# Kernel tuning notes

Measured on AMD Instinct MI355X. Metric: run time of the kernel, lower is better.

The kernel has to match this reference:

```python
import jax, jax.numpy as jnp
import numpy as np

N = 100_000      # nodes
E = 1_600_000    # edges (avg degree 16)
IN_DIM = 256
HID = 128
N_OUT = 2


def _linear_params(key, fan_in, fan_out):
    kw, kb = jax.random.split(key)
    bound = 1.0 / np.sqrt(fan_in)
    W = jax.random.uniform(kw, (fan_in, fan_out), jnp.float32, -bound, bound)
    b = jax.random.uniform(kb, (fan_out,), jnp.float32, -bound, bound)
    return W, b


def setup_inputs() -> dict:
    key = jax.random.key(0)
    ks = jax.random.split(key, 6)
    edge_index = jax.random.randint(ks[0], (2, E), 0, N, dtype=jnp.int64)
    x = jax.random.normal(ks[1], (N, IN_DIM), jnp.float32)
    Wi, bi = _linear_params(ks[2], IN_DIM, HID)   # NodeInitializer.lin
    W1, b1 = _linear_params(ks[3], HID, HID)      # GCNConv 1
    W2, b2 = _linear_params(ks[4], HID, HID)      # GCNConv 2
    Wh, bh = _linear_params(ks[5], HID, N_OUT)    # head
    return {"edge_index": edge_index, "x": x, "Wi": Wi, "bi": bi,
            "W1": W1, "b1": b1, "W2": W2, "b2": b2, "Wh": Wh, "bh": bh}


def reference(edge_index, x, Wi, bi, W1, b1, W2, b2, Wh, bh):
    n = x.shape[0]
    # GCNConv preprocessing: add self-loops, symmetric degree normalization.
    loops = jnp.arange(n, dtype=edge_index.dtype)
    src = jnp.concatenate([edge_index[0], loops])  # message source
    dst = jnp.concatenate([edge_index[1], loops])  # aggregation target
    deg = jax.ops.segment_sum(jnp.ones(src.shape[0], jnp.float32), dst, num_segments=n)
    dinv = jnp.where(deg > 0, deg ** -0.5, 0.0)
    norm = dinv[src] * dinv[dst]                   # [E+N]

    # NodeInitializer: relu(linear(x)); dropout = identity (eval mode)
    h = jax.nn.relu(x @ Wi + bi)

    # Two GCNConv layers (no relu between, matching SimpleGCN.forward)
    for W, b in ((W1, b1), (W2, b2)):
        msg = (h @ W)[src] * norm[:, None]         # gather + normalize, [E+N, HID]
        h = jax.ops.segment_sum(msg, dst, num_segments=n) + b  # scatter-add

    return h @ Wh + bh                             # [N, N_OUT]
```

## Files before the change

kernel.cpp:

```cpp
#include <hip/hip_runtime.h>
#include <hip/hip_bf16.h>

#define N_NODES 100000
#define N_EDGES 1600000
#define DIM_IN  256
#define DIM_H   128

#define NBKT 782
#define CPAD 16
#define EPB  8192
#define NBLK ((N_EDGES + EPB - 1) / EPB)

typedef __attribute__((ext_vector_type(8))) short short8;
typedef __attribute__((ext_vector_type(4))) float f32x4;

__device__ __forceinline__ int get_src(const int* e, int is64, int i) {
  return is64 ? e[2 * i] : e[i];
}
__device__ __forceinline__ int get_dst(const int* e, int is64, int i) {
  return is64 ? e[2 * (N_EDGES + i)] : e[N_EDGES + i];
}

__global__ __launch_bounds__(1024)
void k_init(const int* __restrict__ e, int* __restrict__ flag,
            int* __restrict__ bcnt) {
  if (blockIdx.x == 0) {
    __shared__ int s;
    if (threadIdx.x == 0) s = 0;
    __syncthreads();
    atomicOr(&s, e[2 * threadIdx.x + 1]);
    __syncthreads();
    if (threadIdx.x == 0) *flag = (s == 0) ? 1 : 0;
  } else {
    int i = (blockIdx.x - 1) * 1024 + threadIdx.x;
    if (i < NBKT * CPAD) bcnt[i] = 0;
  }
}

__global__ __launch_bounds__(256) void k_zero(int* __restrict__ p, int n) {
  int i = blockIdx.x * 256 + threadIdx.x;
  if (i < n) p[i] = 0;
}

__global__ __launch_bounds__(1024)
void k_binc(const int* __restrict__ eidx, const int* __restrict__ flag,
            int* __restrict__ bcnt) {
  __shared__ int hist[NBKT];
  const int t = threadIdx.x;
  const int is64 = *flag;
  for (int i = t; i < NBKT; i += 1024) hist[i] = 0;
  __syncthreads();
#pragma unroll
  for (int j = 0; j < EPB / 1024; ++j) {
    int e = blockIdx.x * EPB + j * 1024 + t;
    if (e < N_EDGES) {
      unsigned s = (unsigned)get_src(eidx, is64, e);
      unsigned d = (unsigned)get_dst(eidx, is64, e);
      if (s < N_NODES && d < N_NODES) atomicAdd(&hist[d >> 7], 1);
    }
  }
  __syncthreads();
  for (int i = t; i < NBKT; i += 1024) {
    int h = hist[i];
    if (h) atomicAdd(&bcnt[i * CPAD], h);
  }
}

__global__ __launch_bounds__(1024)
void k_bscan(int* __restrict__ bcnt, int* __restrict__ bbase) {
  __shared__ int sm[1024];
  int t = threadIdx.x;
  int v = (t < NBKT) ? bcnt[t * CPAD] : 0;
  sm[t] = v;
  __syncthreads();
  for (int d = 1; d < 1024; d <<= 1) {
    int u = (t >= d) ? sm[t - d] : 0;
    __syncthreads();
    sm[t] += u;
    __syncthreads();
  }
  if (t < NBKT) {
    int excl = sm[t] - v;
    bbase[t] = excl;
    bcnt[t * CPAD] = excl;
    if (t == NBKT - 1) bbase[NBKT] = sm[t];
  }
}

__global__ __launch_bounds__(1024)
void k_bin(const int* __restrict__ eidx, const int* __restrict__ flag,
           int* __restrict__ bcnt, unsigned* __restrict__ ebuf) {
  __shared__ int hist[NBKT];
  __shared__ int cur[NBKT];
  const int t = threadIdx.x;
  const int is64 = *flag;
  for (int i = t; i < NBKT; i += 1024) hist[i] = 0;
  unsigned rec[EPB / 1024];
  int bkt[EPB / 1024];
  __syncthreads();
#pragma unroll
  for (int j = 0; j < EPB / 1024; ++j) {
    int e = blockIdx.x * EPB + j * 1024 + t;
    bkt[j] = -1;
    rec[j] = 0;
    if (e < N_EDGES) {
      unsigned s = (unsigned)get_src(eidx, is64, e);
      unsigned d = (unsigned)get_dst(eidx, is64, e);
      if (s < N_NODES && d < N_NODES) {
        bkt[j] = (int)(d >> 7);
        rec[j] = s | ((d & 127u) << 17);
        atomicAdd(&hist[bkt[j]], 1);
      }
    }
  }
  __syncthreads();
  for (int i = t; i < NBKT; i += 1024) {
    int h = hist[i];
    cur[i] = h ? atomicAdd(&bcnt[i * CPAD], h) : 0;
  }
  __syncthreads();
#pragma unroll
  for (int j = 0; j < EPB / 1024; ++j) {
    if (bkt[j] >= 0) {
      int pos = atomicAdd(&cur[bkt[j]], 1);
      ebuf[pos] = rec[j];
    }
  }
}

__global__ __launch_bounds__(256)
void k_csr(const int* __restrict__ bbase, const unsigned* __restrict__ ebuf,
           int* __restrict__ off, float* __restrict__ dinv,
           int* __restrict__ csr) {
  __shared__ int hist[128];
  __shared__ int scn[128];
  __shared__ int cur[128];
  const int b = blockIdx.x, t = threadIdx.x;
  const int n0 = b << 7;
  const int start = bbase[b], end = bbase[b + 1];
  if (t < 128) hist[t] = 0;
  __syncthreads();
  for (int i = start + t; i < end; i += 256) {
    atomicAdd(&hist[ebuf[i] >> 17], 1);
  }
  __syncthreads();
  if (t < 128) scn[t] = hist[t];
  __syncthreads();
  for (int d = 1; d < 128; d <<= 1) {
    int u = (t < 128 && t >= d) ? scn[t - d] : 0;
    __syncthreads();
    if (t < 128) scn[t] += u;
    __syncthreads();
  }
  if (t < 128) {
    int node = n0 + t;
    if (node < N_NODES) {
      off[node] = start + scn[t];
      dinv[node] = rsqrtf(1.0f + (float)hist[t]);
      cur[t] = start + scn[t] - hist[t];
    }
  }
  __syncthreads();
  for (int i = start + t; i < end; i += 256) {
    unsigned r = ebuf[i];
    int pos = atomicAdd(&cur[r >> 17], 1);
    csr[pos] = (int)(r & 0x1FFFFu);
  }
}

__device__ __forceinline__ ushort f2bf(float f) {
  unsigned u = __float_as_uint(f);
  unsigned r = (u + 0x7fffu + ((u >> 16) & 1u)) >> 16;
  return (ushort)r;
}
__device__ __forceinline__ float bf2f(ushort h) {
  return __uint_as_float(((unsigned)h) << 16);
}

__device__ __forceinline__ void load8(const float* p, float* o) {
  float4 a = reinterpret_cast<const float4*>(p)[0];
  float4 b = reinterpret_cast<const float4*>(p)[1];
  o[0] = a.x; o[1] = a.y; o[2] = a.z; o[3] = a.w;
  o[4] = b.x; o[5] = b.y; o[6] = b.z; o[7] = b.w;
}

__global__ __launch_bounds__(256)
void k_prep(const float* __restrict__ Wi, const float* __restrict__ W1,
            const float* __restrict__ W2, const float* __restrict__ Wh,
            const float* __restrict__ b1, const float* __restrict__ b2,
            const float* __restrict__ bh, ushort* __restrict__ outHi,
            float* __restrict__ Wcc) {
  __shared__ float Wc2s[DIM_H][2];
  constexpr int CH = DIM_IN / 32;
  if (blockIdx.x == 16) {
    const int t = threadIdx.x;
    const int i = t >> 1, j = t & 1;
    float s = 0.f;
#pragma unroll 4
    for (int m = 0; m < DIM_H; ++m) s += W2[(size_t)i * DIM_H + m] * Wh[m * 2 + j];
    Wc2s[i][j] = s;
    __syncthreads();
    float c = 0.f;
#pragma unroll 4
    for (int k = 0; k < DIM_H; ++k) c += W1[(size_t)i * DIM_H + k] * Wc2s[k][j];
    Wcc[i * 2 + j] = c;
    if (t < 2) {
      float a = 0.f, b = 0.f;
      for (int k = 0; k < DIM_H; ++k) {
        a += b1[k] * Wc2s[k][t];
        b += b2[k] * Wh[k * 2 + t];
      }
      Wcc[256 + t] = a;
      Wcc[258 + t] = b + bh[t];
    }
    return;
  }
  int idx = blockIdx.x * 256 + threadIdx.x;
  int n  = idx & 15;
  int qq = (idx >> 4) & 3;
  int nt = (idx >> 6) & 7;
  int c  = idx >> 9;
  int col = nt * 16 + n;
  short8 h8, l8;
#pragma unroll
  for (int j = 0; j < 8; ++j) {
    float v = Wi[(size_t)(c * 32 + qq * 8 + j) * DIM_H + col];
    ushort hb = f2bf(v);
    ushort lb = f2bf(v - bf2f(hb));
    h8[j] = (short)hb;
    l8[j] = (short)lb;
  }
  ((short8*)outHi)[idx] = h8;
  ((short8*)outHi)[CH * 512 + idx] = l8;
}

template <int K>
__global__ __launch_bounds__(256)
void k_gemm_xz(const float* __restrict__ A, const ushort* __restrict__ Bfrag,
               const float* __restrict__ bias, const float* __restrict__ Wcc,
               const float* __restrict__ dinv, float4* __restrict__ tbl) {
  constexpr int CH = K / 32;
  const int tid = threadIdx.x;
  const int wave = tid >> 6, lane = tid & 63;
  const int m_l = lane & 15, quad = lane >> 4;
  const int mrow = blockIdx.x * 64 + wave * 16;

  f32x4 acc[8];
#pragma unroll
  for (int nt = 0; nt < 8; ++nt) acc[nt] = (f32x4){0.f, 0.f, 0.f, 0.f};

  const short8* Bhi8 = (const short8*)Bfrag;
  const short8* Blo8 = Bhi8 + CH * 512;

  const int rowc = (mrow + m_l < N_NODES) ? (mrow + m_l) : (N_NODES - 1);
  const float* Ap = &A[(size_t)rowc * K + quad * 8];

#pragma unroll 2
  for (int c = 0; c < CH; ++c) {
    float v[8];
    load8(Ap + c * 32, v);
    short8 ahi, alo;
#pragma unroll
    for (int j = 0; j < 8; ++j) {
      ushort hb = f2bf(v[j]);
      ushort lb = f2bf(v[j] - bf2f(hb));
      ahi[j] = (short)hb;
      alo[j] = (short)lb;
    }
#pragma unroll
    for (int nt = 0; nt < 8; ++nt) {
      const int bent = ((c * 8 + nt) * 4 + quad) * 16 + m_l;
      short8 bhi = Bhi8[bent];
      short8 blo = Blo8[bent];
      acc[nt] = __builtin_amdgcn_mfma_f32_16x16x32_bf16(ahi, bhi, acc[nt], 0, 0, 0);
      acc[nt] = __builtin_amdgcn_mfma_f32_16x16x32_bf16(ahi, blo, acc[nt], 0, 0, 0);
      acc[nt] = __builtin_amdgcn_mfma_f32_16x16x32_bf16(alo, bhi, acc[nt], 0, 0, 0);
    }
  }

  float p0[4], p1[4];
#pragma unroll
  for (int r = 0; r < 4; ++r) { p0[r] = 0.f; p1[r] = 0.f; }
#pragma unroll
  for (int nt = 0; nt < 8; ++nt) {
    const int colg = nt * 16 + m_l;
    const float bv = bias[colg];
    const float w0 = Wcc[colg * 2 + 0];
    const float w1 = Wcc[colg * 2 + 1];
#pragma unroll
    for (int r = 0; r < 4; ++r) {
      float hv = fmaxf(acc[nt][r] + bv, 0.f);
      p0[r] += hv * w0;
      p1[r] += hv * w1;
    }
  }
#pragma unroll
  for (int o = 1; o < 16; o <<= 1) {
#pragma unroll
    for (int r = 0; r < 4; ++r) {
      p0[r] += __shfl_xor(p0[r], o);
      p1[r] += __shfl_xor(p1[r], o);
    }
  }
  if (m_l == 0) {
#pragma unroll
    for (int r = 0; r < 4; ++r) {
      const int rowg = mrow + quad * 4 + r;
      if (rowg < N_NODES) {
        float dn = dinv[rowg];
        tbl[rowg] = make_float4(dn * p0[r], dn * p1[r], dn, 0.f);
      }
    }
  }
}

__global__ __launch_bounds__(256)
void k_aggr1(const int* __restrict__ off, const int* __restrict__ csr,
             const float4* __restrict__ tbl, float2* __restrict__ tb2,
             float* __restrict__ g) {
  int node = blockIdx.x * 256 + threadIdx.x;
  if (node >= N_NODES) return;
  int start = (node == 0) ? 0 : off[node - 1];
  int end = off[node];
  float4 self = tbl[node];
  float s0 = self.x, s1 = self.y, sd = self.z;
  int e = start;
  for (; e + 3 < end; e += 4) {
    int i0 = csr[e], i1 = csr[e + 1], i2 = csr[e + 2], i3 = csr[e + 3];
    float4 v0 = tbl[i0];
    float4 v1 = tbl[i1];
    float4 v2 = tbl[i2];
    float4 v3 = tbl[i3];
    s0 += (v0.x + v1.x) + (v2.x + v3.x);
    s1 += (v0.y + v1.y) + (v2.y + v3.y);
    sd += (v0.z + v1.z) + (v2.z + v3.z);
  }
  for (; e < end; ++e) {
    float4 v = tbl[csr[e]];
    s0 += v.x; s1 += v.y; sd += v.z;
  }
  float dn = self.z;
  tb2[node] = make_float2(dn * dn * s0, dn * dn * s1);
  g[node] = dn * sd;
}

__global__ __launch_bounds__(256)
void k_aggr2(const int* __restrict__ off, const int* __restrict__ csr,
             const float2* __restrict__ tb2, const float* __restrict__ dinv,
             const float* __restrict__ g, const float* __restrict__ tail,
             float* __restrict__ out) {
  int node = blockIdx.x * 256 + threadIdx.x;
  if (node >= N_NODES) return;
  int start = (node == 0) ? 0 : off[node - 1];
  int end = off[node];
  float2 self = tb2[node];
  float s0 = self.x, s1 = self.y;
  int e = start;
  for (; e + 3 < end; e += 4) {
    int i0 = csr[e], i1 = csr[e + 1], i2 = csr[e + 2], i3 = csr[e + 3];
    float2 v0 = tb2[i0];
    float2 v1 = tb2[i1];
    float2 v2 = tb2[i2];
    float2 v3 = tb2[i3];
    s0 += (v0.x + v1.x) + (v2.x + v3.x);
    s1 += (v0.y + v1.y) + (v2.y + v3.y);
  }
  for (; e < end; ++e) {
    float2 v = tb2[csr[e]];
    s0 += v.x; s1 += v.y;
  }
  float dn = dinv[node], gv = g[node];
  float o0 = dn * s0 + gv * tail[0] + tail[2];
  float o1 = dn * s1 + gv * tail[1] + tail[3];
  reinterpret_cast<float2*>(out)[node] = make_float2(o0, o1);
}

__global__ __launch_bounds__(256) void k_count(const int* __restrict__ eidx,
                                               const int* __restrict__ flag,
                                               int* __restrict__ off) {
  int e = blockIdx.x * 256 + threadIdx.x;
  int is64 = *flag;
  if (e < N_EDGES) {
    unsigned d = (unsigned)get_dst(eidx, is64, e);
    if (d < N_NODES) atomicAdd(&off[d], 1);
  }
}

__global__ __launch_bounds__(256) void k_dinv_old(const int* __restrict__ off,
                                                  float* __restrict__ dinv) {
  int i = blockIdx.x * 256 + threadIdx.x;
  if (i < N_NODES) dinv[i] = rsqrtf(1.0f + (float)off[i]);
}

template <int K>
__global__ __launch_bounds__(256)
void k_gemm(const float* __restrict__ A, const float* __restrict__ B,
            const float* __restrict__ bias, const float* __restrict__ scale,
            float* __restrict__ C, const int do_relu) {
  __shared__ float As[64][33];
  const int tid = threadIdx.x;
  const int tx = tid & 15;
  const int ty = tid >> 4;
  const int m0 = blockIdx.x * 64;

  float acc[4][8];
#pragma unroll
  for (int i = 0; i < 4; ++i)
#pragma unroll
    for (int j = 0; j < 8; ++j) acc[i][j] = 0.f;

  const int rs = tid >> 2;
  const int ks = (tid & 3) * 8;

  for (int k0 = 0; k0 < K; k0 += 32) {
    float av8[8];
    const int gm = m0 + rs;
    if (gm < N_NODES) {
      load8(&A[(size_t)gm * K + k0 + ks], av8);
    } else {
#pragma unroll
      for (int j = 0; j < 8; ++j) av8[j] = 0.f;
    }
    __syncthreads();
#pragma unroll
    for (int j = 0; j < 8; ++j) As[rs][ks + j] = av8[j];
    __syncthreads();

    const float* Bp = B + (size_t)k0 * DIM_H + tx * 8;
#pragma unroll 4
    for (int k = 0; k < 32; ++k) {
      float bv[8];
      load8(Bp + (size_t)k * DIM_H, bv);
      float av[4];
#pragma unroll
      for (int rr = 0; rr < 4; ++rr) av[rr] = As[ty * 4 + rr][k];
#pragma unroll
      for (int rr = 0; rr < 4; ++rr)
#pragma unroll
        for (int cc = 0; cc < 8; ++cc)
          acc[rr][cc] = fmaf(av[rr], bv[cc], acc[rr][cc]);
    }
  }

  float bs[8];
  if (bias) {
    load8(bias + tx * 8, bs);
  } else {
#pragma unroll
    for (int j = 0; j < 8; ++j) bs[j] = 0.f;
  }
#pragma unroll
  for (int rr = 0; rr < 4; ++rr) {
    const int gm = m0 + ty * 4 + rr;
    if (gm < N_NODES) {
      float sc = scale ? scale[gm] : 1.0f;
      float v[8];
#pragma unroll
      for (int cc = 0; cc < 8; ++cc) {
        float t = acc[rr][cc] + bs[cc];
        if (do_relu) t = fmaxf(t, 0.f);
        v[cc] = t * sc;
      }
      float* Cp = &C[(size_t)gm * DIM_H + tx * 8];
      reinterpret_cast<float4*>(Cp)[0] = make_float4(v[0], v[1], v[2], v[3]);
      reinterpret_cast<float4*>(Cp)[1] = make_float4(v[4], v[5], v[6], v[7]);
    }
  }
}

__global__ __launch_bounds__(256)
void k_aggr_init(const float* __restrict__ t, const float* __restrict__ dinv,
                 const float* __restrict__ bias, float* __restrict__ h) {
  int idx = blockIdx.x * 256 + threadIdx.x;
  if (idx < N_NODES * DIM_H) {
    int i = idx >> 7;
    int c = idx & 127;
    float d = dinv[i];
    h[idx] = bias[c] + t[idx] * d * d;
  }
}

__global__ __launch_bounds__(256)
void k_aggr_edges(const int* __restrict__ eidx, const int* __restrict__ flag,
                  const float* __restrict__ t, const float* __restrict__ dinv,
                  float* __restrict__ h) {
  int e = blockIdx.x * 2 + (threadIdx.x >> 7);
  int c = threadIdx.x & 127;
  int is64 = *flag;
  if (e < N_EDGES) {
    unsigned s = (unsigned)get_src(eidx, is64, e);
    unsigned d = (unsigned)get_dst(eidx, is64, e);
    if (s < N_NODES && d < N_NODES) {
      float nrm = dinv[s] * dinv[d];
      unsafeAtomicAdd(&h[(size_t)d * DIM_H + c], t[(size_t)s * DIM_H + c] * nrm);
    }
  }
}

__global__ __launch_bounds__(256)
void k_head_f32(const float* __restrict__ h, const float* __restrict__ Wh,
                const float* __restrict__ bh, float* __restrict__ out) {
  int node = blockIdx.x * 4 + (threadIdx.x >> 6);
  int lane = threadIdx.x & 63;
  if (node >= N_NODES) return;
  float h0 = h[(size_t)node * DIM_H + lane];
  float h1 = h[(size_t)node * DIM_H + 64 + lane];
  float s0 = h0 * Wh[lane * 2 + 0] + h1 * Wh[(lane + 64) * 2 + 0];
  float s1 = h0 * Wh[lane * 2 + 1] + h1 * Wh[(lane + 64) * 2 + 1];
#pragma unroll
  for (int off = 32; off > 0; off >>= 1) {
    s0 += __shfl_down(s0, off);
    s1 += __shfl_down(s1, off);
  }
  if (lane == 0) {
    reinterpret_cast<float2*>(out)[node] = make_float2(s0 + bh[0], s1 + bh[1]);
  }
}

extern "C" void kernel_launch(void* const* d_in, const int* in_sizes, int n_in,
                              void* d_out, int out_size, void* d_ws, size_t ws_size,
                              hipStream_t stream) {
  (void)in_sizes; (void)n_in; (void)out_size;
  const int* eidx = (const int*)d_in[0];
  const float* x  = (const float*)d_in[1];
  const float* Wi = (const float*)d_in[2];
  const float* bi = (const float*)d_in[3];
  const float* W1 = (const float*)d_in[4];
  const float* b1 = (const float*)d_in[5];
  const float* W2 = (const float*)d_in[6];
  const float* b2 = (const float*)d_in[7];
  const float* Wh = (const float*)d_in[8];
  const float* bh = (const float*)d_in[9];
  float* out = (float*)d_out;

  const int gE  = (N_EDGES + 255) / 256;
  const int gM  = (N_NODES + 63) / 64;
  const int gW  = (N_NODES + 3) / 4;
  const int gN256 = (N_NODES + 255) / 256;

  char* ws = (char*)d_ws;
  int* flag = (int*)ws;

  const size_t need1 = 17410048;

  if (ws_size >= need1) {
    int*      bcnt  = (int*)(ws + 4096);
    int*      bbase = (int*)(ws + 57344);
    float*    Wcc   = (float*)(ws + 61440);
    ushort*   bfWi  = (ushort*)(ws + 65536);
    int*      off   = (int*)(ws + 262144);
    float*    dinv  = (float*)(ws + 720896);
    float*    g     = (float*)(ws + 1179648);
    float4*   tbl   = (float4*)(ws + 1638400);
    float2*   tb2   = (float2*)(ws + 3407872);
    int*      csr   = (int*)(ws + 4456448);
    unsigned* ebuf  = (unsigned*)(ws + 11010048);

    k_init<<<1 + (NBKT * CPAD + 1023) / 1024, 1024, 0, stream>>>(eidx, flag, bcnt);
    k_binc<<<NBLK, 1024, 0, stream>>>(eidx, flag, bcnt);
    k_bscan<<<1, 1024, 0, stream>>>(bcnt, bbase);
    k_bin<<<NBLK, 1024, 0, stream>>>(eidx, flag, bcnt, ebuf);
    k_csr<<<NBKT, 256, 0, stream>>>(bbase, ebuf, off, dinv, csr);

    k_prep<<<17, 256, 0, stream>>>(Wi, W1, W2, Wh, b1, b2, bh, bfWi, Wcc);

    k_gemm_xz<DIM_IN><<<gM, 256, 0, stream>>>(x, bfWi, bi, Wcc, dinv, tbl);
    k_aggr1<<<gN256, 256, 0, stream>>>(off, csr, tbl, tb2, g);
    k_aggr2<<<gN256, 256, 0, stream>>>(off, csr, tb2, dinv, g, Wcc + 256, out);
  } else {
    const int gN  = (N_NODES + 255) / 256;
    int*   off  = (int*)(ws + 4096);
    float* dinv = (float*)(ws + 404480);
    float* fbA  = (float*)(ws + 804864);
    float* fbB  = (float*)(ws + 804864 + (size_t)N_NODES * DIM_H * 4);
    const int gNH = (N_NODES * DIM_H + 255) / 256;
    const int gE2 = (N_EDGES + 1) / 2;
    k_init<<<1, 1024, 0, stream>>>(eidx, flag, (int*)(ws + 4096));
    k_zero<<<gN, 256, 0, stream>>>(off, N_NODES);
    k_count<<<gE, 256, 0, stream>>>(eidx, flag, off);
    k_dinv_old<<<gN, 256, 0, stream>>>(off, dinv);

    k_gemm<DIM_IN><<<gM, 256, 0, stream>>>(x, Wi, bi, nullptr, fbA, 1);
    k_gemm<DIM_H><<<gM, 256, 0, stream>>>(fbA, W1, nullptr, nullptr, fbB, 0);
    k_aggr_init<<<gNH, 256, 0, stream>>>(fbB, dinv, b1, fbA);
    k_aggr_edges<<<gE2, 256, 0, stream>>>(eidx, flag, fbB, dinv, fbA);
    k_gemm<DIM_H><<<gM, 256, 0, stream>>>(fbA, W2, nullptr, nullptr, fbB, 0);
    k_aggr_init<<<gNH, 256, 0, stream>>>(fbB, dinv, b2, fbA);
    k_aggr_edges<<<gE2, 256, 0, stream>>>(eidx, flag, fbB, dinv, fbA);
    k_head_f32<<<gW, 256, 0, stream>>>(fbA, Wh, bh, out);
  }
}
```

Baseline: 302.4 us.

## Restructure x@Wi GEMM: 128-row tiles, LDS double-buffered A, per-wave column split

Result: faster. 294.5 us (-2.6%).

```diff
diff --git a/kernel.cpp b/kernel.cpp
--- a/kernel.cpp
+++ b/kernel.cpp
@@ -182,6 +182,16 @@
   float4 b = reinterpret_cast<const float4*>(p)[1];
   o[0] = a.x; o[1] = a.y; o[2] = a.z; o[3] = a.w;
   o[4] = b.x; o[5] = b.y; o[6] = b.z; o[7] = b.w;
+}
+
+__device__ __forceinline__ void cvt_split(const float* v, short8& h, short8& l) {
+#pragma unroll
+  for (int j = 0; j < 8; ++j) {
+    ushort hb = f2bf(v[j]);
+    ushort lb = f2bf(v[j] - bf2f(hb));
+    h[j] = (short)hb;
+    l[j] = (short)lb;
+  }
 }
 
 __global__ __launch_bounds__(256)
@@ -235,81 +245,136 @@
 }
 
 template <int K>
-__global__ __launch_bounds__(256)
+__global__ __launch_bounds__(256, 3)
 void k_gemm_xz(const float* __restrict__ A, const ushort* __restrict__ Bfrag,
                const float* __restrict__ bias, const float* __restrict__ Wcc,
                const float* __restrict__ dinv, float4* __restrict__ tbl) {
   constexpr int CH = K / 32;
+  __shared__ __align__(16) ushort AhiS[2][512 * 8];
+  __shared__ __align__(16) ushort AloS[2][512 * 8];
   const int tid = threadIdx.x;
+  const int m0 = blockIdx.x * 128;
   const int wave = tid >> 6, lane = tid & 63;
   const int m_l = lane & 15, quad = lane >> 4;
-  const int mrow = blockIdx.x * 64 + wave * 16;
-
-  f32x4 acc[8];
-#pragma unroll
-  for (int nt = 0; nt < 8; ++nt) acc[nt] = (f32x4){0.f, 0.f, 0.f, 0.f};
+  const int rs = tid >> 2, q = tid & 3;
+
+  f32x4 acc[2][8];
+#pragma unroll
+  for (int i = 0; i < 2; ++i)
+#pragma unroll
+    for (int j = 0; j < 8; ++j) acc[i][j] = (f32x4){0.f, 0.f, 0.f, 0.f};
 
   const short8* Bhi8 = (const short8*)Bfrag;
   const short8* Blo8 = Bhi8 + CH * 512;
-
-  const int rowc = (mrow + m_l < N_NODES) ? (mrow + m_l) : (N_NODES - 1);
-  const float* Ap = &A[(size_t)rowc * K + quad * 8];
-
-#pragma unroll 2
+  short8* Ah = (short8*)AhiS;
+  short8* Al = (short8*)AloS;
+
+  const int gr0 = m0 + rs, gr1 = m0 + rs + 64;
+  const float* Ap0 = &A[(size_t)((gr0 < N_NODES) ? gr0 : (N_NODES - 1)) * K + q * 8];
+  const float* Ap1 = &A[(size_t)((gr1 < N_NODES) ? gr1 : (N_NODES - 1)) * K + q * 8];
+  const int ent0 = (rs >> 4) * 64 + q * 16 + (rs & 15);
+  const int ent1 = ent0 + 256;
+
+  {
+    float v0[8], v1[8];
+    load8(Ap0, v0);
+    load8(Ap1, v1);
+    short8 h, l;
+    cvt_split(v0, h, l);
+    Ah[ent0] = h; Al[ent0] = l;
+    cvt_split(v1, h, l);
+    Ah[ent1] = h; Al[ent1] = l;
+  }
+  __syncthreads();
+
+#pragma unroll
   for (int c = 0; c < CH; ++c) {
-    float v[8];
-    load8(Ap + c * 32, v);
-    short8 ahi, alo;
-#pragma unroll
-    for (int j = 0; j < 8; ++j) {
-      ushort hb = f2bf(v[j]);
-      ushort lb = f2bf(v[j] - bf2f(hb));
-      ahi[j] = (short)hb;
-      alo[j] = (short)lb;
-    }
-#pragma unroll
-    for (int nt = 0; nt < 8; ++nt) {
-      const int bent = ((c * 8 + nt) * 4 + quad) * 16 + m_l;
-      short8 bhi = Bhi8[bent];
-      short8 blo = Blo8[bent];
-      acc[nt] = __builtin_amdgcn_mfma_f32_16x16x32_bf16(ahi, bhi, acc[nt], 0, 0, 0);
-      acc[nt] = __builtin_amdgcn_mfma_f32_16x16x32_bf16(ahi, blo, acc[nt], 0, 0, 0);
-      acc[nt] = __builtin_amdgcn_mfma_f32_16x16x32_bf16(alo, bhi, acc[nt], 0, 0, 0);
-    }
-  }
-
-  float p0[4], p1[4];
-#pragma unroll
-  for (int r = 0; r < 4; ++r) { p0[r] = 0.f; p1[r] = 0.f; }
-#pragma unroll
-  for (int nt = 0; nt < 8; ++nt) {
-    const int colg = nt * 16 + m_l;
+    const int cur = c & 1, nxt = cur ^ 1;
+    float v0n[8], v1n[8];
+    if (c + 1 < CH) {
+      load8(Ap0 + (c + 1) * 32, v0n);
+      load8(Ap1 + (c + 1) * 32, v1n);
+    }
+    const int bent0 = ((c * 8 + wave * 2 + 0) * 4 + quad) * 16 + m_l;
+    const int bent1 = ((c * 8 + wave * 2 + 1) * 4 + quad) * 16 + m_l;
+    short8 bhi0 = Bhi8[bent0], blo0 = Blo8[bent0];
+    short8 bhi1 = Bhi8[bent1], blo1 = Blo8[bent1];
+    const short8* AhC = Ah + cur * 512;
+    const short8* AlC = Al + cur * 512;
+#pragma unroll
+    for (int mt = 0; mt < 8; ++mt) {
+      short8 ahi = AhC[mt * 64 + quad * 16 + m_l];
+      short8 alo = AlC[mt * 64 + quad * 16 + m_l];
+      acc[0][mt] = __builtin_amdgcn_mfma_f32_16x16x32_bf16(ahi, bhi0, acc[0][mt], 0, 0, 0);
+      acc[0][mt] = __builtin_amdgcn_mfma_f32_16x16x32_bf16(ahi, blo0, acc[0][mt], 0, 0, 0);
+      acc[0][mt] = __builtin_amdgcn_mfma_f32_16x16x32_bf16(alo, bhi0, acc[0][mt], 0, 0, 0);
+      acc[1][mt] = __builtin_amdgcn_mfma_f32_16x16x32_bf16(ahi, bhi1, acc[1][mt], 0, 0, 0);
+      acc[1][mt] = __builtin_amdgcn_mfma_f32_16x16x32_bf16(ahi, blo1, acc[1][mt], 0, 0, 0);
+      acc[1][mt] = __builtin_amdgcn_mfma_f32_16x16x32_bf16(alo, bhi1, acc[1][mt], 0, 0, 0);
+    }
+    if (c + 1 < CH) {
+      short8 h, l;
+      cvt_split(v0n, h, l);
+      Ah[nxt * 512 + ent0] = h; Al[nxt * 512 + ent0] = l;
+      cvt_split(v1n, h, l);
+      Ah[nxt * 512 + ent1] = h; Al[nxt * 512 + ent1] = l;
+    }
+    __syncthreads();
+  }
+
+  float p0[8][4], p1[8][4];
+#pragma unroll
+  for (int mt = 0; mt < 8; ++mt)
+#pragma unroll
+    for (int r = 0; r < 4; ++r) { p0[mt][r] = 0.f; p1[mt][r] = 0.f; }
+#pragma unroll
+  for (int ntl = 0; ntl < 2; ++ntl) {
+    const int colg = (wave * 2 + ntl) * 16 + m_l;
     const float bv = bias[colg];
     const float w0 = Wcc[colg * 2 + 0];
     const float w1 = Wcc[colg * 2 + 1];
 #pragma unroll
-    for (int r = 0; r < 4; ++r) {
-      float hv = fmaxf(acc[nt][r] + bv, 0.f);
-      p0[r] += hv * w0;
-      p1[r] += hv * w1;
-    }
+    for (int mt = 0; mt < 8; ++mt)
+#pragma unroll
+      for (int r = 0; r < 4; ++r) {
+        float hv = fmaxf(acc[ntl][mt][r] + bv, 0.f);
+        p0[mt][r] += hv * w0;
+        p1[mt][r] += hv * w1;
+      }
   }
 #pragma unroll
   for (int o = 1; o < 16; o <<= 1) {
 #pragma unroll
-    for (int r = 0; r < 4; ++r) {
-      p0[r] += __shfl_xor(p0[r], o);
-      p1[r] += __shfl_xor(p1[r], o);
-    }
-  }
+    for (int mt = 0; mt < 8; ++mt)
+#pragma unroll
+      for (int r = 0; r < 4; ++r) {
+        p0[mt][r] += __shfl_xor(p0[mt][r], o);
+        p1[mt][r] += __shfl_xor(p1[mt][r], o);
+      }
+  }
+  float* zred = (float*)AhiS;
   if (m_l == 0) {
 #pragma unroll
-    for (int r = 0; r < 4; ++r) {
-      const int rowg = mrow + quad * 4 + r;
-      if (rowg < N_NODES) {
-        float dn = dinv[rowg];
-        tbl[rowg] = make_float4(dn * p0[r], dn * p1[r], dn, 0.f);
+    for (int mt = 0; mt < 8; ++mt)
+#pragma unroll
+      for (int r = 0; r < 4; ++r) {
+        zred[(((0 * 4 + wave) * 4 + quad) * 8 + mt) * 4 + r] = p0[mt][r];
+        zred[(((1 * 4 + wave) * 4 + quad) * 8 + mt) * 4 + r] = p1[mt][r];
       }
+  }
+  __syncthreads();
+  if (tid < 128) {
+    const int mt = tid >> 4, qd = (tid >> 2) & 3, r = tid & 3;
+    const int rowg = m0 + tid;
+    if (rowg < N_NODES) {
+      float s0 = 0.f, s1 = 0.f;
+#pragma unroll
+      for (int w = 0; w < 4; ++w) {
+        s0 += zred[(((0 * 4 + w) * 4 + qd) * 8 + mt) * 4 + r];
+        s1 += zred[(((1 * 4 + w) * 4 + qd) * 8 + mt) * 4 + r];
+      }
+      float dn = dinv[rowg];
+      tbl[rowg] = make_float4(dn * s0, dn * s1, dn, 0.f);
     }
   }
 }
@@ -535,6 +600,7 @@
 
   const int gE  = (N_EDGES + 255) / 256;
   const int gM  = (N_NODES + 63) / 64;
+  const int gM2 = (N_NODES + 127) / 128;
   const int gW  = (N_NODES + 3) / 4;
   const int gN256 = (N_NODES + 255) / 256;
 
@@ -564,7 +630,7 @@
 
     k_prep<<<17, 256, 0, stream>>>(Wi, W1, W2, Wh, b1, b2, bh, bfWi, Wcc);
 
-    k_gemm_xz<DIM_IN><<<gM, 256, 0, stream>>>(x, bfWi, bi, Wcc, dinv, tbl);
+    k_gemm_xz<DIM_IN><<<gM2, 256, 0, stream>>>(x, bfWi, bi, Wcc, dinv, tbl);
     k_aggr1<<<gN256, 256, 0, stream>>>(off, csr, tbl, tb2, g);
     k_aggr2<<<gN256, 256, 0, stream>>>(off, csr, tb2, dinv, g, Wcc + 256, out);
   } else {
```
